# Kernel tuning notes

Measured on AMD Instinct MI355X. Metric: run time of the kernel, lower is better.

## Reference

```python
import jax, jax.numpy as jnp
import numpy as np

NUM_CLASSES = 1000
K_PROTOS = 5
FEAT_DIM = 1024
BATCH = 16384


def _l2norm(x, axis=-1, eps=1e-12):
    # matches torch.nn.functional.normalize
    n = jnp.linalg.norm(x, axis=axis, keepdims=True)
    return x / jnp.maximum(n, eps)


def setup_inputs() -> dict:
    key = jax.random.key(0)
    k1, k2, k3 = jax.random.split(key, 3)
    z = jax.random.normal(k1, (BATCH, FEAT_DIM), dtype=jnp.float32)
    y = jax.random.randint(k2, (BATCH,), 0, NUM_CLASSES, dtype=jnp.int64)
    # learned prototype bank, dense [C, K, D] (all slots populated)
    P = jax.random.normal(k3, (NUM_CLASSES, K_PROTOS, FEAT_DIM), dtype=jnp.float32)
    return {"z": z, "y": y, "P": P}


def reference(z, y, P):
    """Returns (pos_sim [B], neg_sim [B]): max cosine sim to same-class and
    other-class prototypes respectively (PrototypeBank.forward)."""
    C, K, D = P.shape
    z_n = _l2norm(z)                     # [B, D]
    P_n = _l2norm(P).reshape(C * K, D)   # [C*K, D]
    sim = jnp.einsum('bd,pd->bp', z_n, P_n)  # [B, C*K]
    proto_labels = jnp.repeat(jnp.arange(C, dtype=y.dtype), K)  # [C*K]
    same = proto_labels[None, :] == y[:, None]  # [B, C*K]
    neg_inf = jnp.asarray(-jnp.inf, sim.dtype)
    pos_sim = jnp.max(jnp.where(same, sim, neg_inf), axis=1)
    neg_sim = jnp.max(jnp.where(same, neg_inf, sim), axis=1)
    return pos_sim, neg_sim
```

## Files before the change

### kernel.cpp

```cpp
#include <hip/hip_runtime.h>
#include <hip/hip_bf16.h>
#include <stdint.h>

#define BATCH 16384
#define D 1024
#define NCLS 1000
#define NPROTO 5000
#define NPROTO_PAD 5120
#define BM 64
#define NCH 5
#define NKT 32
#define KSTRIDE (320 * 64 * 8)

typedef float f32x4 __attribute__((ext_vector_type(4)));
typedef __bf16 bf16x8 __attribute__((ext_vector_type(8)));

__device__ __forceinline__ unsigned short f2bf(float x) {
    unsigned u = __float_as_uint(x);
    u += 0x7FFFu + ((u >> 16) & 1u);
    return (unsigned short)(u >> 16);
}

__global__ __launch_bounds__(256) void k_prep(
        const float* __restrict__ z, const float* __restrict__ P,
        unsigned short* __restrict__ zb, unsigned short* __restrict__ pbf) {
    const int b = blockIdx.x;
    const int t = threadIdx.x;
    const int e0 = 4 * t;
    const float* src = nullptr;
    unsigned short* dst;
    if (b < BATCH) {
        src = z + (size_t)b * D;
        dst = zb + (size_t)b * D + e0;
    } else {
        const int r = b - BATCH;
        const int kt = e0 >> 5;
        const int lk = (e0 >> 3) & 3;
        const int ke = e0 & 7;
        dst = pbf + (((size_t)kt * 320 + (r >> 4)) * 64 + (r & 15) + 16 * lk) * 8 + ke;
        if (r < NPROTO) src = P + (size_t)r * D;
    }
    if (src == nullptr) {
        *(ushort4*)dst = make_ushort4(0, 0, 0, 0);
        return;
    }
    float4 v = ((const float4*)src)[t];
    float ss = v.x * v.x + v.y * v.y + v.z * v.z + v.w * v.w;
    #pragma unroll
    for (int o = 32; o >= 1; o >>= 1) ss += __shfl_xor(ss, o);
    __shared__ float red[4];
    const int wave = t >> 6;
    if ((t & 63) == 0) red[wave] = ss;
    __syncthreads();
    const float s = red[0] + red[1] + red[2] + red[3];
    const float inv = 1.0f / fmaxf(sqrtf(s), 1e-12f);
    ushort4 o4;
    o4.x = f2bf(v.x * inv); o4.y = f2bf(v.y * inv);
    o4.z = f2bf(v.z * inv); o4.w = f2bf(v.w * inv);
    *(ushort4*)dst = o4;
}

#define MM(A, B, C) __builtin_amdgcn_mfma_f32_16x16x32_bf16(A, B, C, 0, 0, 0)

__global__ __launch_bounds__(1024, 4) void k_gemm(
        const unsigned short* __restrict__ zb,
        const unsigned short* __restrict__ pbf,
        const int* __restrict__ y,
        float* __restrict__ out) {
    __shared__ __align__(16) unsigned short LA[NKT][4][64][8];
    __shared__ float redP[16][64];
    __shared__ float redN[16][64];

    const int t = threadIdx.x;
    const int w = t >> 6;
    const int lane = t & 63;
    const int lm = lane & 15, lk = lane >> 4;
    const int rowbase = blockIdx.x * BM;

    redP[t >> 6][t & 63] = -INFINITY;
    redN[t >> 6][t & 63] = -INFINITY;

    {
        const int ktw = lane >> 1;
        const int lk0 = (lane & 1) * 2;
        #pragma unroll
        for (int j = 0; j < 4; ++j) {
            const int r = w * 4 + j;
            const unsigned short* gp = zb + (size_t)(rowbase + r) * D + lane * 16;
            const bf16x8 v0 = *(const bf16x8*)gp;
            const bf16x8 v1 = *(const bf16x8*)(gp + 8);
            *(bf16x8*)&LA[ktw][r >> 4][(r & 15) + 16 * lk0][0] = v0;
            *(bf16x8*)&LA[ktw][r >> 4][(r & 15) + 16 * (lk0 + 1)][0] = v1;
        }
    }
    __syncthreads();

    #pragma unroll 1
    for (int c = 0; c < NCH; ++c) {
        const int grp0 = c * 64 + w * 4;
        const unsigned short* pB = pbf + ((size_t)grp0 * 64 + lane) * 8;

        f32x4 acc[4][4];
        #pragma unroll
        for (int mi = 0; mi < 4; ++mi)
            #pragma unroll
            for (int ni = 0; ni < 4; ++ni) {
                f32x4 z4 = {0.0f, 0.0f, 0.0f, 0.0f};
                acc[mi][ni] = z4;
            }

        #pragma unroll 1
        for (int kt = 0; kt < NKT; ++kt) {
            const unsigned short* q = pB + (size_t)kt * KSTRIDE;
            const bf16x8 b0 = *(const bf16x8*)(q);
            const bf16x8 b1 = *(const bf16x8*)(q + 512);
            const bf16x8 b2 = *(const bf16x8*)(q + 1024);
            const bf16x8 b3 = *(const bf16x8*)(q + 1536);
            const bf16x8 a0 = *(const bf16x8*)&LA[kt][0][lane][0];
            const bf16x8 a1 = *(const bf16x8*)&LA[kt][1][lane][0];
            const bf16x8 a2 = *(const bf16x8*)&LA[kt][2][lane][0];
            const bf16x8 a3 = *(const bf16x8*)&LA[kt][3][lane][0];
            acc[0][0] = MM(a0, b0, acc[0][0]);
            acc[0][1] = MM(a0, b1, acc[0][1]);
            acc[0][2] = MM(a0, b2, acc[0][2]);
            acc[0][3] = MM(a0, b3, acc[0][3]);
            acc[1][0] = MM(a1, b0, acc[1][0]);
            acc[1][1] = MM(a1, b1, acc[1][1]);
            acc[1][2] = MM(a1, b2, acc[1][2]);
            acc[1][3] = MM(a1, b3, acc[1][3]);
            acc[2][0] = MM(a2, b0, acc[2][0]);
            acc[2][1] = MM(a2, b1, acc[2][1]);
            acc[2][2] = MM(a2, b2, acc[2][2]);
            acc[2][3] = MM(a2, b3, acc[2][3]);
            acc[3][0] = MM(a3, b0, acc[3][0]);
            acc[3][1] = MM(a3, b1, acc[3][1]);
            acc[3][2] = MM(a3, b2, acc[3][2]);
            acc[3][3] = MM(a3, b3, acc[3][3]);
        }

        #pragma unroll
        for (int mi = 0; mi < 4; ++mi) {
            #pragma unroll
            for (int r = 0; r < 4; ++r) {
                const int row = mi * 16 + lk * 4 + r;
                const unsigned yv = (unsigned)y[rowbase + row];
                float pm = -INFINITY, nm = -INFINITY;
                #pragma unroll
                for (int ni = 0; ni < 4; ++ni) {
                    const unsigned col = (unsigned)(c * 1024 + w * 64 + ni * 16 + lm);
                    const unsigned lbl = __umulhi(col, 0xCCCCCCCDu) >> 2;
                    const float v = acc[mi][ni][r];
                    const bool same = (lbl == yv);
                    pm = same ? fmaxf(pm, v) : pm;
                    nm = (!same && col < NPROTO) ? fmaxf(nm, v) : nm;
                }
                #pragma unroll
                for (int off = 1; off < 16; off <<= 1) {
                    pm = fmaxf(pm, __shfl_xor(pm, off));
                    nm = fmaxf(nm, __shfl_xor(nm, off));
                }
                if (lm == 0) {
                    redP[w][row] = fmaxf(redP[w][row], pm);
                    redN[w][row] = fmaxf(redN[w][row], nm);
                }
            }
        }
    }

    __syncthreads();
    if (t < 64) {
        float p = redP[0][t], n = redN[0][t];
        #pragma unroll
        for (int ww = 1; ww < 16; ++ww) {
            p = fmaxf(p, redP[ww][t]);
            n = fmaxf(n, redN[ww][t]);
        }
        out[rowbase + t] = p;
        out[BATCH + rowbase + t] = n;
    }
}

extern "C" void kernel_launch(void* const* d_in, const int* in_sizes, int n_in,
                              void* d_out, int out_size, void* d_ws, size_t ws_size,
                              hipStream_t stream) {
    const float* z = (const float*)d_in[0];
    const int*   y = (const int*)d_in[1];
    const float* P = (const float*)d_in[2];

    unsigned short* zb = (unsigned short*)d_ws;
    unsigned short* pbf = zb + (size_t)BATCH * D;
    float* out = (float*)d_out;

    k_prep<<<BATCH + NPROTO_PAD, 256, 0, stream>>>(z, P, zb, pbf);
    k_gemm<<<BATCH / BM, 1024, 0, stream>>>(zb, pbf, y, out);
}
```

Baseline: 181.1 us.

## Switch GEMM to 32x32x16 MFMA with matching layouts and register prefetch of B

Replaces the 16x16x32 bf16 MFMA tiling with 32x32x16 MFMA instructions. The prototype and LDS A-tile layouts are reorganised to fit the new operand fragments, and the epilogue reduction is remapped to the 32x32 output layout. The k-loop is unrolled by two and software-pipelined so the next B fragments are loaded from global memory while the current MFMAs run. The aim is fewer instructions and better hiding of global-load latency. The cost is a wider cross-lane shuffle reduction in the epilogue and possibly more register pressure.

Result: slower. 228.9 us (+26.4%).

```diff
diff --git a/kernel.cpp b/kernel.cpp
--- a/kernel.cpp
+++ b/kernel.cpp
@@ -10,9 +10,10 @@
 #define BM 64
 #define NCH 5
 #define NKT 32
-#define KSTRIDE (320 * 64 * 8)
-
-typedef float f32x4 __attribute__((ext_vector_type(4)));
+#define KS_SLAB 81920
+#define KT_STRIDE 163840
+
+typedef float f32x16 __attribute__((ext_vector_type(16)));
 typedef __bf16 bf16x8 __attribute__((ext_vector_type(8)));
 
 __device__ __forceinline__ unsigned short f2bf(float x) {
@@ -35,9 +36,11 @@
     } else {
         const int r = b - BATCH;
         const int kt = e0 >> 5;
-        const int lk = (e0 >> 3) & 3;
-        const int ke = e0 & 7;
-        dst = pbf + (((size_t)kt * 320 + (r >> 4)) * 64 + (r & 15) + 16 * lk) * 8 + ke;
+        const int ks = (e0 >> 4) & 1;
+        const int khalf = (e0 >> 3) & 1;
+        const int e = e0 & 7;
+        dst = pbf + ((((size_t)kt * 2 + ks) * 160 + (r >> 5)) * 64 +
+                     (r & 31) + 32 * khalf) * 8 + e;
         if (r < NPROTO) src = P + (size_t)r * D;
     }
     if (src == nullptr) {
@@ -60,94 +63,120 @@
     *(ushort4*)dst = o4;
 }
 
-#define MM(A, B, C) __builtin_amdgcn_mfma_f32_16x16x32_bf16(A, B, C, 0, 0, 0)
+#define MM32(A, B, C) __builtin_amdgcn_mfma_f32_32x32x16_bf16(A, B, C, 0, 0, 0)
 
 __global__ __launch_bounds__(1024, 4) void k_gemm(
         const unsigned short* __restrict__ zb,
         const unsigned short* __restrict__ pbf,
         const int* __restrict__ y,
         float* __restrict__ out) {
-    __shared__ __align__(16) unsigned short LA[NKT][4][64][8];
+    __shared__ __align__(16) unsigned short LA[NKT][2][2][64][8];
     __shared__ float redP[16][64];
     __shared__ float redN[16][64];
 
     const int t = threadIdx.x;
     const int w = t >> 6;
     const int lane = t & 63;
-    const int lm = lane & 15, lk = lane >> 4;
+    const int cl = lane & 31;
+    const int hi = lane >> 5;
     const int rowbase = blockIdx.x * BM;
 
     redP[t >> 6][t & 63] = -INFINITY;
     redN[t >> 6][t & 63] = -INFINITY;
 
     {
-        const int ktw = lane >> 1;
-        const int lk0 = (lane & 1) * 2;
+        const int kt = lane >> 1;
+        const int ks = lane & 1;
         #pragma unroll
         for (int j = 0; j < 4; ++j) {
             const int r = w * 4 + j;
             const unsigned short* gp = zb + (size_t)(rowbase + r) * D + lane * 16;
             const bf16x8 v0 = *(const bf16x8*)gp;
             const bf16x8 v1 = *(const bf16x8*)(gp + 8);
-            *(bf16x8*)&LA[ktw][r >> 4][(r & 15) + 16 * lk0][0] = v0;
-            *(bf16x8*)&LA[ktw][r >> 4][(r & 15) + 16 * (lk0 + 1)][0] = v1;
+            const int rt = r >> 5;
+            *(bf16x8*)&LA[kt][ks][rt][r & 31][0] = v0;
+            *(bf16x8*)&LA[kt][ks][rt][(r & 31) + 32][0] = v1;
         }
     }
     __syncthreads();
 
     #pragma unroll 1
     for (int c = 0; c < NCH; ++c) {
-        const int grp0 = c * 64 + w * 4;
-        const unsigned short* pB = pbf + ((size_t)grp0 * 64 + lane) * 8;
-
-        f32x4 acc[4][4];
-        #pragma unroll
-        for (int mi = 0; mi < 4; ++mi)
+        const int grp0 = c * 32 + w * 2;
+        const unsigned short* pB = pbf + (size_t)grp0 * 512 + lane * 8;
+
+        f32x16 acc[2][2];
+        #pragma unroll
+        for (int mi = 0; mi < 2; ++mi)
             #pragma unroll
-            for (int ni = 0; ni < 4; ++ni) {
-                f32x4 z4 = {0.0f, 0.0f, 0.0f, 0.0f};
-                acc[mi][ni] = z4;
-            }
+            for (int ni = 0; ni < 2; ++ni)
+                #pragma unroll
+                for (int e = 0; e < 16; ++e)
+                    acc[mi][ni][e] = 0.0f;
+
+        bf16x8 bc0 = *(const bf16x8*)(pB);
+        bf16x8 bc1 = *(const bf16x8*)(pB + 512);
+        bf16x8 bc2 = *(const bf16x8*)(pB + KS_SLAB);
+        bf16x8 bc3 = *(const bf16x8*)(pB + KS_SLAB + 512);
+        bf16x8 bn0, bn1, bn2, bn3;
 
         #pragma unroll 1
-        for (int kt = 0; kt < NKT; ++kt) {
-            const unsigned short* q = pB + (size_t)kt * KSTRIDE;
-            const bf16x8 b0 = *(const bf16x8*)(q);
-            const bf16x8 b1 = *(const bf16x8*)(q + 512);
-            const bf16x8 b2 = *(const bf16x8*)(q + 1024);
-            const bf16x8 b3 = *(const bf16x8*)(q + 1536);
-            const bf16x8 a0 = *(const bf16x8*)&LA[kt][0][lane][0];
-            const bf16x8 a1 = *(const bf16x8*)&LA[kt][1][lane][0];
-            const bf16x8 a2 = *(const bf16x8*)&LA[kt][2][lane][0];
-            const bf16x8 a3 = *(const bf16x8*)&LA[kt][3][lane][0];
-            acc[0][0] = MM(a0, b0, acc[0][0]);
-            acc[0][1] = MM(a0, b1, acc[0][1]);
-            acc[0][2] = MM(a0, b2, acc[0][2]);
-            acc[0][3] = MM(a0, b3, acc[0][3]);
-            acc[1][0] = MM(a1, b0, acc[1][0]);
-            acc[1][1] = MM(a1, b1, acc[1][1]);
-            acc[1][2] = MM(a1, b2, acc[1][2]);
-            acc[1][3] = MM(a1, b3, acc[1][3]);
-            acc[2][0] = MM(a2, b0, acc[2][0]);
-            acc[2][1] = MM(a2, b1, acc[2][1]);
-            acc[2][2] = MM(a2, b2, acc[2][2]);
-            acc[2][3] = MM(a2, b3, acc[2][3]);
-            acc[3][0] = MM(a3, b0, acc[3][0]);
-            acc[3][1] = MM(a3, b1, acc[3][1]);
-            acc[3][2] = MM(a3, b2, acc[3][2]);
-            acc[3][3] = MM(a3, b3, acc[3][3]);
-        }
-
-        #pragma unroll
-        for (int mi = 0; mi < 4; ++mi) {
+        for (int kt = 0; kt < NKT; kt += 2) {
+            {
+                const unsigned short* q = pB + (size_t)(kt + 1) * KT_STRIDE;
+                bn0 = *(const bf16x8*)(q);
+                bn1 = *(const bf16x8*)(q + 512);
+                bn2 = *(const bf16x8*)(q + KS_SLAB);
+                bn3 = *(const bf16x8*)(q + KS_SLAB + 512);
+            }
+            {
+                const bf16x8 a00 = *(const bf16x8*)&LA[kt][0][0][lane][0];
+                const bf16x8 a01 = *(const bf16x8*)&LA[kt][0][1][lane][0];
+                acc[0][0] = MM32(a00, bc0, acc[0][0]);
+                acc[0][1] = MM32(a00, bc1, acc[0][1]);
+                acc[1][0] = MM32(a01, bc0, acc[1][0]);
+                acc[1][1] = MM32(a01, bc1, acc[1][1]);
+                const bf16x8 a10 = *(const bf16x8*)&LA[kt][1][0][lane][0];
+                const bf16x8 a11 = *(const bf16x8*)&LA[kt][1][1][lane][0];
+                acc[0][0] = MM32(a10, bc2, acc[0][0]);
+                acc[0][1] = MM32(a10, bc3, acc[0][1]);
+                acc[1][0] = MM32(a11, bc2, acc[1][0]);
+                acc[1][1] = MM32(a11, bc3, acc[1][1]);
+            }
+            {
+                const int ktn = (kt + 2 < NKT) ? kt + 2 : NKT - 1;
+                const unsigned short* q = pB + (size_t)ktn * KT_STRIDE;
+                bc0 = *(const bf16x8*)(q);
+                bc1 = *(const bf16x8*)(q + 512);
+                bc2 = *(const bf16x8*)(q + KS_SLAB);
+                bc3 = *(const bf16x8*)(q + KS_SLAB + 512);
+            }
+            {
+                const bf16x8 a00 = *(const bf16x8*)&LA[kt + 1][0][0][lane][0];
+                const bf16x8 a01 = *(const bf16x8*)&LA[kt + 1][0][1][lane][0];
+                acc[0][0] = MM32(a00, bn0, acc[0][0]);
+                acc[0][1] = MM32(a00, bn1, acc[0][1]);
+                acc[1][0] = MM32(a01, bn0, acc[1][0]);
+                acc[1][1] = MM32(a01, bn1, acc[1][1]);
+                const bf16x8 a10 = *(const bf16x8*)&LA[kt + 1][1][0][lane][0];
+                const bf16x8 a11 = *(const bf16x8*)&LA[kt + 1][1][1][lane][0];
+                acc[0][0] = MM32(a10, bn2, acc[0][0]);
+                acc[0][1] = MM32(a10, bn3, acc[0][1]);
+                acc[1][0] = MM32(a11, bn2, acc[1][0]);
+                acc[1][1] = MM32(a11, bn3, acc[1][1]);
+            }
+        }
+
+        #pragma unroll
+        for (int mi = 0; mi < 2; ++mi) {
             #pragma unroll
-            for (int r = 0; r < 4; ++r) {
-                const int row = mi * 16 + lk * 4 + r;
+            for (int r = 0; r < 16; ++r) {
+                const int row = mi * 32 + (r & 3) + 8 * (r >> 2) + 4 * hi;
                 const unsigned yv = (unsigned)y[rowbase + row];
                 float pm = -INFINITY, nm = -INFINITY;
                 #pragma unroll
-                for (int ni = 0; ni < 4; ++ni) {
-                    const unsigned col = (unsigned)(c * 1024 + w * 64 + ni * 16 + lm);
+                for (int ni = 0; ni < 2; ++ni) {
+                    const unsigned col = (unsigned)(c * 1024 + w * 64 + ni * 32 + cl);
                     const unsigned lbl = __umulhi(col, 0xCCCCCCCDu) >> 2;
                     const float v = acc[mi][ni][r];
                     const bool same = (lbl == yv);
@@ -155,11 +184,11 @@
                     nm = (!same && col < NPROTO) ? fmaxf(nm, v) : nm;
                 }
                 #pragma unroll
-                for (int off = 1; off < 16; off <<= 1) {
+                for (int off = 1; off < 32; off <<= 1) {
                     pm = fmaxf(pm, __shfl_xor(pm, off));
                     nm = fmaxf(nm, __shfl_xor(nm, off));
                 }
-                if (lm == 0) {
+                if (cl == 0) {
                     redP[w][row] = fmaxf(redP[w][row], pm);
                     redN[w][row] = fmaxf(redN[w][row], nm);
                 }
```

## Retile GEMM to 128-row blocks split over column halves with double-buffered LDS staging

Applied to the files above, without the earlier changes.

Stores the z activations in an MFMA-fragment layout and stages them into LDS with global_load_lds, double-buffered over K windows so loads overlap MFMA work. Each block now covers 128 rows and half of the prototype columns. This doubles reuse of each B-fragment load per block. The two column-half partial maxima go to a workspace and are merged by a new finish kernel. It also raises wave priority around the MFMA bursts, at the cost of an extra launch and more barriers per chunk.

Result: slower. 222.3 us (+22.7%).

```diff
diff --git a/kernel.cpp b/kernel.cpp
--- a/kernel.cpp
+++ b/kernel.cpp
@@ -7,10 +7,14 @@
 #define NCLS 1000
 #define NPROTO 5000
 #define NPROTO_PAD 5120
-#define BM 64
+#define NGRP 320
+#define NRGRP 1024
+#define BM 128
+#define COLHALF 2560
 #define NCH 5
 #define NKT 32
-#define KSTRIDE (320 * 64 * 8)
+#define KT_B (NGRP * 512)
+#define KT_A (NRGRP * 512)
 
 typedef float f32x4 __attribute__((ext_vector_type(4)));
 typedef __bf16 bf16x8 __attribute__((ext_vector_type(8)));
@@ -23,21 +27,21 @@
 
 __global__ __launch_bounds__(256) void k_prep(
         const float* __restrict__ z, const float* __restrict__ P,
-        unsigned short* __restrict__ zb, unsigned short* __restrict__ pbf) {
+        unsigned short* __restrict__ abf, unsigned short* __restrict__ pbf) {
     const int b = blockIdx.x;
     const int t = threadIdx.x;
     const int e0 = 4 * t;
+    const int kt = e0 >> 5;
+    const int lk = (e0 >> 3) & 3;
+    const int e = e0 & 7;
     const float* src = nullptr;
     unsigned short* dst;
     if (b < BATCH) {
         src = z + (size_t)b * D;
-        dst = zb + (size_t)b * D + e0;
+        dst = abf + (((size_t)kt * NRGRP + (b >> 4)) * 64 + (b & 15) + 16 * lk) * 8 + e;
     } else {
         const int r = b - BATCH;
-        const int kt = e0 >> 5;
-        const int lk = (e0 >> 3) & 3;
-        const int ke = e0 & 7;
-        dst = pbf + (((size_t)kt * 320 + (r >> 4)) * 64 + (r & 15) + 16 * lk) * 8 + ke;
+        dst = pbf + (((size_t)kt * NGRP + (r >> 4)) * 64 + (r & 15) + 16 * lk) * 8 + e;
         if (r < NPROTO) src = P + (size_t)r * D;
     }
     if (src == nullptr) {
@@ -60,45 +64,53 @@
     *(ushort4*)dst = o4;
 }
 
+#define GLL(gp, lp) __builtin_amdgcn_global_load_lds( \
+    (__attribute__((address_space(1))) const unsigned int*)(const void*)(gp), \
+    (__attribute__((address_space(3))) unsigned int*)(void*)(lp), 16, 0, 0)
+
 #define MM(A, B, C) __builtin_amdgcn_mfma_f32_16x16x32_bf16(A, B, C, 0, 0, 0)
 
 __global__ __launch_bounds__(1024, 4) void k_gemm(
-        const unsigned short* __restrict__ zb,
+        const unsigned short* __restrict__ abf,
         const unsigned short* __restrict__ pbf,
         const int* __restrict__ y,
-        float* __restrict__ out) {
-    __shared__ __align__(16) unsigned short LA[NKT][4][64][8];
+        float* __restrict__ outP, float* __restrict__ outN) {
+    __shared__ __align__(16) unsigned short LA[2][8][8][64][8];
     __shared__ float redP[16][64];
     __shared__ float redN[16][64];
 
     const int t = threadIdx.x;
-    const int w = t >> 6;
-    const int lane = t & 63;
+    const int w = t >> 6, lane = t & 63;
     const int lm = lane & 15, lk = lane >> 4;
-    const int rowbase = blockIdx.x * BM;
-
-    redP[t >> 6][t & 63] = -INFINITY;
-    redN[t >> 6][t & 63] = -INFINITY;
-
-    {
-        const int ktw = lane >> 1;
-        const int lk0 = (lane & 1) * 2;
-        #pragma unroll
-        for (int j = 0; j < 4; ++j) {
-            const int r = w * 4 + j;
-            const unsigned short* gp = zb + (size_t)(rowbase + r) * D + lane * 16;
-            const bf16x8 v0 = *(const bf16x8*)gp;
-            const bf16x8 v1 = *(const bf16x8*)(gp + 8);
-            *(bf16x8*)&LA[ktw][r >> 4][(r & 15) + 16 * lk0][0] = v0;
-            *(bf16x8*)&LA[ktw][r >> 4][(r & 15) + 16 * (lk0 + 1)][0] = v1;
-        }
-    }
+    const int wh = w >> 3;
+    const int wc = w & 7;
+    const int bid = blockIdx.x;
+    const int rowbase = (bid >> 1) * BM;
+    const int ch = bid & 1;
+    const int rb16 = rowbase >> 4;
+
+    redP[w][lane] = -INFINITY;
+    redN[w][lane] = -INFINITY;
+
+    const unsigned short* aw = abf + ((size_t)(rb16 + wc)) * 512 + lane * 8;
+
+#define STAGE(BUF, WIN) do {                                                 \
+    _Pragma("unroll")                                                        \
+    for (int j_ = 0; j_ < 4; ++j_) {                                         \
+        const int s_ = 2 * j_ + wh;                                          \
+        GLL(aw + (size_t)((WIN) * 8 + s_) * KT_A, &LA[BUF][s_][wc][0][0]);   \
+    }                                                                        \
+} while (0)
+
+    STAGE(0, 0);
+    asm volatile("s_waitcnt vmcnt(0)" ::: "memory");
     __syncthreads();
 
+    int buf = 0;
     #pragma unroll 1
     for (int c = 0; c < NCH; ++c) {
-        const int grp0 = c * 64 + w * 4;
-        const unsigned short* pB = pbf + ((size_t)grp0 * 64 + lane) * 8;
+        const unsigned short* pBc =
+            pbf + (size_t)(ch * 160 + c * 32 + wc * 4) * 512 + lane * 8;
 
         f32x4 acc[4][4];
         #pragma unroll
@@ -110,32 +122,43 @@
             }
 
         #pragma unroll 1
-        for (int kt = 0; kt < NKT; ++kt) {
-            const unsigned short* q = pB + (size_t)kt * KSTRIDE;
-            const bf16x8 b0 = *(const bf16x8*)(q);
-            const bf16x8 b1 = *(const bf16x8*)(q + 512);
-            const bf16x8 b2 = *(const bf16x8*)(q + 1024);
-            const bf16x8 b3 = *(const bf16x8*)(q + 1536);
-            const bf16x8 a0 = *(const bf16x8*)&LA[kt][0][lane][0];
-            const bf16x8 a1 = *(const bf16x8*)&LA[kt][1][lane][0];
-            const bf16x8 a2 = *(const bf16x8*)&LA[kt][2][lane][0];
-            const bf16x8 a3 = *(const bf16x8*)&LA[kt][3][lane][0];
-            acc[0][0] = MM(a0, b0, acc[0][0]);
-            acc[0][1] = MM(a0, b1, acc[0][1]);
-            acc[0][2] = MM(a0, b2, acc[0][2]);
-            acc[0][3] = MM(a0, b3, acc[0][3]);
-            acc[1][0] = MM(a1, b0, acc[1][0]);
-            acc[1][1] = MM(a1, b1, acc[1][1]);
-            acc[1][2] = MM(a1, b2, acc[1][2]);
-            acc[1][3] = MM(a1, b3, acc[1][3]);
-            acc[2][0] = MM(a2, b0, acc[2][0]);
-            acc[2][1] = MM(a2, b1, acc[2][1]);
-            acc[2][2] = MM(a2, b2, acc[2][2]);
-            acc[2][3] = MM(a2, b3, acc[2][3]);
-            acc[3][0] = MM(a3, b0, acc[3][0]);
-            acc[3][1] = MM(a3, b1, acc[3][1]);
-            acc[3][2] = MM(a3, b2, acc[3][2]);
-            acc[3][3] = MM(a3, b3, acc[3][3]);
+        for (int win = 0; win < 4; ++win) {
+            if (!(c == NCH - 1 && win == 3)) STAGE(buf ^ 1, (win + 1) & 3);
+
+            #pragma unroll 1
+            for (int k8 = 0; k8 < 8; ++k8) {
+                const int kt = win * 8 + k8;
+                const unsigned short* q = pBc + (size_t)kt * KT_B;
+                const bf16x8 b0 = *(const bf16x8*)(q);
+                const bf16x8 b1 = *(const bf16x8*)(q + 512);
+                const bf16x8 b2 = *(const bf16x8*)(q + 1024);
+                const bf16x8 b3 = *(const bf16x8*)(q + 1536);
+                const bf16x8 a0 = *(const bf16x8*)&LA[buf][k8][wh * 4 + 0][lane][0];
+                const bf16x8 a1 = *(const bf16x8*)&LA[buf][k8][wh * 4 + 1][lane][0];
+                const bf16x8 a2 = *(const bf16x8*)&LA[buf][k8][wh * 4 + 2][lane][0];
+                const bf16x8 a3 = *(const bf16x8*)&LA[buf][k8][wh * 4 + 3][lane][0];
+                __builtin_amdgcn_s_setprio(1);
+                acc[0][0] = MM(a0, b0, acc[0][0]);
+                acc[0][1] = MM(a0, b1, acc[0][1]);
+                acc[0][2] = MM(a0, b2, acc[0][2]);
+                acc[0][3] = MM(a0, b3, acc[0][3]);
+                acc[1][0] = MM(a1, b0, acc[1][0]);
+                acc[1][1] = MM(a1, b1, acc[1][1]);
+                acc[1][2] = MM(a1, b2, acc[1][2]);
+                acc[1][3] = MM(a1, b3, acc[1][3]);
+                acc[2][0] = MM(a2, b0, acc[2][0]);
+                acc[2][1] = MM(a2, b1, acc[2][1]);
+                acc[2][2] = MM(a2, b2, acc[2][2]);
+                acc[2][3] = MM(a2, b3, acc[2][3]);
+                acc[3][0] = MM(a3, b0, acc[3][0]);
+                acc[3][1] = MM(a3, b1, acc[3][1]);
+                acc[3][2] = MM(a3, b2, acc[3][2]);
+                acc[3][3] = MM(a3, b3, acc[3][3]);
+                __builtin_amdgcn_s_setprio(0);
+            }
+            asm volatile("s_waitcnt vmcnt(0)" ::: "memory");
+            __syncthreads();
+            buf ^= 1;
         }
 
         #pragma unroll
@@ -143,11 +166,12 @@
             #pragma unroll
             for (int r = 0; r < 4; ++r) {
                 const int row = mi * 16 + lk * 4 + r;
-                const unsigned yv = (unsigned)y[rowbase + row];
+                const unsigned yv = (unsigned)y[rowbase + wh * 64 + row];
                 float pm = -INFINITY, nm = -INFINITY;
                 #pragma unroll
                 for (int ni = 0; ni < 4; ++ni) {
-                    const unsigned col = (unsigned)(c * 1024 + w * 64 + ni * 16 + lm);
+                    const unsigned col =
+                        (unsigned)(ch * COLHALF + c * 512 + wc * 64 + ni * 16 + lm);
                     const unsigned lbl = __umulhi(col, 0xCCCCCCCDu) >> 2;
                     const float v = acc[mi][ni][r];
                     const bool same = (lbl == yv);
@@ -168,15 +192,27 @@
     }
 
     __syncthreads();
-    if (t < 64) {
-        float p = redP[0][t], n = redN[0][t];
+    if (t < 128) {
+        const int h = t >> 6, rr = t & 63;
+        float p = redP[h * 8][rr], n = redN[h * 8][rr];
         #pragma unroll
-        for (int ww = 1; ww < 16; ++ww) {
-            p = fmaxf(p, redP[ww][t]);
-            n = fmaxf(n, redN[ww][t]);
+        for (int i = 1; i < 8; ++i) {
+            p = fmaxf(p, redP[h * 8 + i][rr]);
+            n = fmaxf(n, redN[h * 8 + i][rr]);
         }
-        out[rowbase + t] = p;
-        out[BATCH + rowbase + t] = n;
+        outP[(size_t)ch * BATCH + rowbase + t] = p;
+        outN[(size_t)ch * BATCH + rowbase + t] = n;
+    }
+#undef STAGE
+}
+
+__global__ __launch_bounds__(256) void k_finish(
+        const float* __restrict__ outP, const float* __restrict__ outN,
+        float* __restrict__ out) {
+    const int i = blockIdx.x * 256 + threadIdx.x;
+    if (i < BATCH) {
+        out[i] = fmaxf(outP[i], outP[BATCH + i]);
+        out[BATCH + i] = fmaxf(outN[i], outN[BATCH + i]);
     }
 }
 
@@ -187,10 +223,13 @@
     const int*   y = (const int*)d_in[1];
     const float* P = (const float*)d_in[2];
 
-    unsigned short* zb = (unsigned short*)d_ws;
-    unsigned short* pbf = zb + (size_t)BATCH * D;
+    unsigned short* abf = (unsigned short*)d_ws;
+    unsigned short* pbf = abf + (size_t)NKT * KT_A;
+    float* outP = (float*)(pbf + (size_t)NKT * KT_B);
+    float* outN = outP + 2 * BATCH;
     float* out = (float*)d_out;
 
-    k_prep<<<BATCH + NPROTO_PAD, 256, 0, stream>>>(z, P, zb, pbf);
-    k_gemm<<<BATCH / BM, 1024, 0, stream>>>(zb, pbf, y, out);
-}
+    k_prep<<<BATCH + NPROTO_PAD, 256, 0, stream>>>(z, P, abf, pbf);
+    k_gemm<<<256, 1024, 0, stream>>>(abf, pbf, y, outP, outN);
+    k_finish<<<(BATCH + 255) / 256, 256, 0, stream>>>(outP, outN, out);
+}
```
